# Performance work log

Hardware: AMD Instinct MI355X
Metric: run time of the kernel (lower is better)

Reference implementation:

```python
import jax, jax.numpy as jnp
import numpy as np
from jax import lax

TOP_K = 8

B, S, D, N, R = 32, 128, 512, 131072, 16


def setup_inputs() -> dict:
    key = jax.random.key(0)
    ks = jax.random.split(key, 10)
    return {
        "query": jax.random.normal(ks[0], (B, S, D), jnp.float32),
        "base_memory": jax.random.normal(ks[1], (N, D), jnp.float32) * 0.01,
        "lora_A": jax.random.normal(ks[2], (N, R), jnp.float32) * 0.01,
        "lora_B": jax.random.normal(ks[3], (R, D), jnp.float32) * 0.01,
        "gru_w_ih": jax.random.normal(ks[4], (3 * D, D), jnp.float32) * 0.02,
        "gru_w_hh": jax.random.normal(ks[5], (3 * D, D), jnp.float32) * 0.02,
        "gru_b_ih": jax.random.normal(ks[6], (3 * D,), jnp.float32) * 0.02,
        "gru_b_hh": jax.random.normal(ks[7], (3 * D,), jnpp.float32) if False else jax.random.normal(ks[7], (3 * D,), jnp.float32) * 0.02,
        "wg_w": jax.random.normal(ks[8], (1, D), jnp.float32) * 0.02,
        "wg_b": jnp.zeros((1,), jnp.float32),
    }


def gru_cell(x, h, w_ih, w_hh, b_ih, b_hh):
    # torch.nn.GRUCell math; gates ordered [r, z, n]
    gx = x @ w_ih.T + b_ih            # [B, 3D]
    gh = h @ w_hh.T + b_hh            # [B, 3D]
    gx_r, gx_z, gx_n = jnp.split(gx, 3, axis=-1)
    gh_r, gh_z, gh_n = jnp.split(gh, 3, axis=-1)
    r = jax.nn.sigmoid(gx_r + gh_r)
    z = jax.nn.sigmoid(gx_z + gh_z)
    n = jnp.tanh(gx_n + r * gh_n)
    return (1.0 - z) * n + z * h


def reference(query, base_memory, lora_A, lora_B, gru_w_ih, gru_w_hh, gru_b_ih, gru_b_hh, wg_w, wg_b):
    mem = base_memory + lora_A @ lora_B                 # [N, D]
    q = query.mean(axis=1)                              # [B, D]
    scores = q @ mem.T                                  # [B, N]
    top_scores, top_idx = lax.top_k(scores, TOP_K)      # [B, K]
    retrieved = mem[top_idx]                            # [B, K, D] gather

    h0 = jnp.zeros_like(q)
    hidden = gru_cell(retrieved.sum(axis=1), h0, gru_w_ih, gru_w_hh, gru_b_ih, gru_b_hh)

    write_prob = jax.nn.sigmoid(hidden @ wg_w.T + wg_b)  # [B, 1]
    value = q                                            # value[b, 0] in torch == q[b]

    # Sequential over batch (matches torch loop order); within a batch the
    # top-k indices are distinct so a vectorized scatter-set is exact.
    def step(m, inp):
        idx, p, v = inp                                  # [K], scalar, [D]
        rows = (1.0 - p) * m[idx] + p * v
        return m.at[idx].set(rows), None

    new_mem, _ = lax.scan(step, base_memory, (top_idx, write_prob[:, 0], value))
    return retrieved, hidden, new_mem
```

## Files before the change

### kernel.cpp

```cpp
#include <hip/hip_runtime.h>
#include <math.h>

#define NROWS 131072
#define DDIM  512
#define BB    32
#define SS    128
#define KK    8

__global__ __launch_bounds__(256) void k_qmean(const float* __restrict__ query,
                                               float* __restrict__ q) {
  __shared__ float part[256];
  int b  = blockIdx.x >> 3;
  int dc = blockIdx.x & 7;
  int t  = threadIdx.x;
  int lane = t & 63;
  int p    = t >> 6;
  const float* src = query + (size_t)b * SS * DDIM + (size_t)(p * 32) * DDIM
                   + dc * 64 + lane;
  float s = 0.f;
  #pragma unroll 8
  for (int i = 0; i < 32; ++i) s += src[(size_t)i * DDIM];
  part[t] = s;
  __syncthreads();
  if (t < 64) {
    float tot = part[t] + part[64 + t] + part[128 + t] + part[192 + t];
    q[b * DDIM + dc * 64 + t] = tot * (1.0f / 128.0f);
  }
}

__global__ __launch_bounds__(256) void k_memscores(const float* __restrict__ base,
                                                   const float* __restrict__ A,
                                                   const float* __restrict__ Bm,
                                                   const float* __restrict__ q,
                                                   float* __restrict__ newmem,
                                                   float* __restrict__ scores) {
  __shared__ float4 sq[4096];
  int t = threadIdx.x;
  const float4* qg = (const float4*)q;
  #pragma unroll
  for (int u = 0; u < 16; ++u) sq[u * 256 + t] = qg[u * 256 + t];
  __syncthreads();

  int r = blockIdx.x * 256 + t;

  const float* Ar = A + (size_t)r * 16;
  float av[16];
  #pragma unroll
  for (int j = 0; j < 4; ++j) {
    float4 a = *(const float4*)(Ar + 4 * j);
    av[4 * j]     = a.x; av[4 * j + 1] = a.y;
    av[4 * j + 2] = a.z; av[4 * j + 3] = a.w;
  }

  float acc[32];
  #pragma unroll
  for (int b = 0; b < 32; ++b) acc[b] = 0.f;

  const float4* brow = (const float4*)(base + (size_t)r * DDIM);
  float4*       nrow = (float4*)(newmem + (size_t)r * DDIM);

  float4 cur0 = brow[0], cur1 = brow[1], cur2 = brow[2], cur3 = brow[3];

  for (int g = 0; g < 32; ++g) {
    int nb = (g < 31) ? 4 * (g + 1) : 0;
    float4 nxt0 = brow[nb];
    float4 nxt1 = brow[nb + 1];
    float4 nxt2 = brow[nb + 2];
    float4 nxt3 = brow[nb + 3];

    #pragma unroll
    for (int j = 0; j < 4; ++j) {
      int d4 = 4 * g + j;
      float4 m = (j == 0) ? cur0 : (j == 1) ? cur1 : (j == 2) ? cur2 : cur3;
      #pragma unroll
      for (int rr = 0; rr < 16; ++rr) {
        float4 bv = *(const float4*)(Bm + rr * DDIM + 4 * d4);
        m.x += av[rr] * bv.x; m.y += av[rr] * bv.y;
        m.z += av[rr] * bv.z; m.w += av[rr] * bv.w;
      }
      nrow[d4] = m;
      #pragma unroll
      for (int b = 0; b < 32; ++b) {
        float4 qv = sq[b * 128 + d4];
        acc[b] += qv.x * m.x + qv.y * m.y + qv.z * m.z + qv.w * m.w;
      }
    }
    cur0 = nxt0; cur1 = nxt1; cur2 = nxt2; cur3 = nxt3;
  }

  #pragma unroll
  for (int b = 0; b < 32; ++b) scores[(size_t)b * NROWS + r] = acc[b];
}

__device__ __forceinline__ void insert8(float (&v)[8], int (&ix)[8], float x, int i) {
  bool better = (x > v[7]) || (x == v[7] && i < ix[7]);
  if (!better) return;
  v[7] = x; ix[7] = i;
  #pragma unroll
  for (int u = 7; u > 0; --u) {
    bool sw = (v[u] > v[u-1]) || (v[u] == v[u-1] && ix[u] < ix[u-1]);
    if (sw) {
      float tv = v[u]; v[u] = v[u-1]; v[u-1] = tv;
      int ti = ix[u]; ix[u] = ix[u-1]; ix[u-1] = ti;
    }
  }
}

__global__ __launch_bounds__(256) void k_topk1(const float* __restrict__ scores,
                                               float* __restrict__ cval,
                                               int* __restrict__ cidx) {
  __shared__ float lval[256][8]; __shared__ int lidx[256][8];
  __shared__ float mval[32][8];  __shared__ int midx[32][8];
  int b = blockIdx.x >> 4, j = blockIdx.x & 15, t = threadIdx.x;
  const float4* s4 = (const float4*)(scores + (size_t)b * NROWS + j * 8192);

  float v[8]; int ix[8];
  #pragma unroll
  for (int e = 0; e < 8; ++e) { v[e] = -1e30f; ix[e] = 0x7fffffff; }
  #pragma unroll
  for (int i = 0; i < 8; ++i) {
    int f4 = i * 256 + t;
    float4 x = s4[f4];
    int n0 = j * 8192 + f4 * 4;
    insert8(v, ix, x.x, n0);
    insert8(v, ix, x.y, n0 + 1);
    insert8(v, ix, x.z, n0 + 2);
    insert8(v, ix, x.w, n0 + 3);
  }
  #pragma unroll
  for (int e = 0; e < 8; ++e) { lval[t][e] = v[e]; lidx[t][e] = ix[e]; }
  __syncthreads();

  if (t < 32) {
    float mv[8]; int mi[8];
    #pragma unroll
    for (int e = 0; e < 8; ++e) { mv[e] = -1e30f; mi[e] = 0x7fffffff; }
    for (int u = 0; u < 8; ++u) {
      int src = t * 8 + u;
      #pragma unroll
      for (int e = 0; e < 8; ++e) insert8(mv, mi, lval[src][e], lidx[src][e]);
    }
    #pragma unroll
    for (int e = 0; e < 8; ++e) { mval[t][e] = mv[e]; midx[t][e] = mi[e]; }
  }
  __syncthreads();

  if (t == 0) {
    float mv[8]; int mi[8];
    #pragma unroll
    for (int e = 0; e < 8; ++e) { mv[e] = -1e30f; mi[e] = 0x7fffffff; }
    for (int u = 0; u < 32; ++u)
      #pragma unroll
      for (int e = 0; e < 8; ++e) insert8(mv, mi, mval[u][e], midx[u][e]);
    #pragma unroll
    for (int e = 0; e < 8; ++e) {
      cval[(b * 16 + j) * 8 + e] = mv[e];
      cidx[(b * 16 + j) * 8 + e] = mi[e];
    }
  }
}

__global__ __launch_bounds__(128) void k_gather(const float* __restrict__ mem,
                                                const float* __restrict__ cval,
                                                const int* __restrict__ cidx,
                                                int* __restrict__ topidx,
                                                float* __restrict__ retrieved,
                                                float* __restrict__ x) {
  __shared__ float scv[128]; __shared__ int sci[128];
  __shared__ int stop[8];
  int b = blockIdx.x, t = threadIdx.x;
  scv[t] = cval[b * 128 + t];
  sci[t] = cidx[b * 128 + t];
  __syncthreads();
  if (t == 0) {
    float mv[8]; int mi[8];
    #pragma unroll
    for (int e = 0; e < 8; ++e) { mv[e] = -1e30f; mi[e] = 0x7fffffff; }
    for (int u = 0; u < 128; ++u) insert8(mv, mi, scv[u], sci[u]);
    #pragma unroll
    for (int e = 0; e < 8; ++e) { stop[e] = mi[e]; topidx[b * 8 + e] = mi[e]; }
  }
  __syncthreads();

  float4 xs = make_float4(0.f, 0.f, 0.f, 0.f);
  #pragma unroll
  for (int k = 0; k < 8; ++k) {
    int row = stop[k];
    float4 vv = *(const float4*)(mem + (size_t)row * DDIM + 4 * t);
    *(float4*)(retrieved + (size_t)(b * 8 + k) * DDIM + 4 * t) = vv;
    xs.x += vv.x; xs.y += vv.y; xs.z += vv.z; xs.w += vv.w;
  }
  *(float4*)(x + (size_t)b * DDIM + 4 * t) = xs;
}

__global__ __launch_bounds__(512) void k_gru(const float* __restrict__ x,
                                             const float* __restrict__ wih,
                                             const float* __restrict__ bih,
                                             const float* __restrict__ bhh,
                                             const float* __restrict__ wgw,
                                             const float* __restrict__ wgb,
                                             float* __restrict__ hidden,
                                             float* __restrict__ pws) {
  __shared__ float sx[512];
  __shared__ float sred[8];
  int b = blockIdx.x, t = threadIdx.x;
  sx[t] = x[b * 512 + t];
  __syncthreads();
  const float* wr = wih + (size_t)t * 512;
  const float* wz = wih + (size_t)(512 + t) * 512;
  const float* wn = wih + (size_t)(1024 + t) * 512;
  float gr = 0.f, gz = 0.f, gn = 0.f;
  #pragma unroll 4
  for (int d4 = 0; d4 < 128; ++d4) {
    float4 xv = *(const float4*)(sx + 4 * d4);
    float4 a = *(const float4*)(wr + 4 * d4);
    float4 c = *(const float4*)(wz + 4 * d4);
    float4 e = *(const float4*)(wn + 4 * d4);
    gr += a.x*xv.x + a.y*xv.y + a.z*xv.z + a.w*xv.w;
    gz += c.x*xv.x + c.y*xv.y + c.z*xv.z + c.w*xv.w;
    gn += e.x*xv.x + e.y*xv.y + e.z*xv.z + e.w*xv.w;
  }
  float r = 1.f / (1.f + expf(-(gr + bih[t]        + bhh[t])));
  float z = 1.f / (1.f + expf(-(gz + bih[512 + t]  + bhh[512 + t])));
  float n = tanhf(gn + bih[1024 + t] + r * bhh[1024 + t]);
  float h = (1.f - z) * n;
  hidden[b * 512 + t] = h;

  float pw = h * wgw[t];
  #pragma unroll
  for (int off = 32; off > 0; off >>= 1) pw += __shfl_down(pw, off, 64);
  if ((t & 63) == 0) sred[t >> 6] = pw;
  __syncthreads();
  if (t == 0) {
    float ssum = 0.f;
    #pragma unroll
    for (int j = 0; j < 8; ++j) ssum += sred[j];
    pws[b] = 1.f / (1.f + expf(-(ssum + wgb[0])));
  }
}

__global__ __launch_bounds__(256) void k_scatter(float* __restrict__ newmem,
                                                 const int* __restrict__ topidx,
                                                 const float* __restrict__ pws,
                                                 const float* __restrict__ q) {
  int t = threadIdx.x;
  int d = blockIdx.x * 64 + (t & 63);
  int k0 = t >> 6;
  for (int b = 0; b < 32; ++b) {
    float p = pws[b];
    float qv = q[b * 512 + d];
    #pragma unroll
    for (int kk = 0; kk < 2; ++kk) {
      int k = k0 + kk * 4;
      int row = topidx[b * 8 + k];
      size_t off = (size_t)row * 512 + d;
      float m = __hip_atomic_load(newmem + off, __ATOMIC_RELAXED,
                                  __HIP_MEMORY_SCOPE_AGENT);
      __hip_atomic_store(newmem + off, (1.f - p) * m + p * qv,
                         __ATOMIC_RELAXED, __HIP_MEMORY_SCOPE_AGENT);
    }
    __syncthreads();
  }
}

extern "C" void kernel_launch(void* const* d_in, const int* in_sizes, int n_in,
                              void* d_out, int out_size, void* d_ws, size_t ws_size,
                              hipStream_t stream) {
  const float* query = (const float*)d_in[0];
  const float* base  = (const float*)d_in[1];
  const float* lA    = (const float*)d_in[2];
  const float* lB    = (const float*)d_in[3];
  const float* wih   = (const float*)d_in[4];
  const float* bih   = (const float*)d_in[6];
  const float* bhh   = (const float*)d_in[7];
  const float* wgw   = (const float*)d_in[8];
  const float* wgb   = (const float*)d_in[9];

  float* out = (float*)d_out;
  float* retrieved = out;
  float* hidden    = out + 131072;
  float* newmem    = out + 147456;

  float* wq  = (float*)d_ws;
  float* wsc = wq + 16384;
  float* wx  = wsc + 4194304;
  float* wp  = wx + 16384;
  int*   wti = (int*)(wp + 32);
  float* wcv = (float*)(wti + 256);
  int*   wci = (int*)(wcv + 4096);

  k_qmean    <<<256, 256, 0, stream>>>(query, wq);
  k_memscores<<<512, 256, 0, stream>>>(base, lA, lB, wq, newmem, wsc);
  k_topk1    <<<512, 256, 0, stream>>>(wsc, wcv, wci);
  k_gather   <<<32,  128, 0, stream>>>(newmem, wcv, wci, wti, retrieved, wx);
  k_gru      <<<32,  512, 0, stream>>>(wx, wih, bih, bhh, wgw, wgb, hidden, wp);
  k_scatter  <<<8,   256, 0, stream>>>(newmem, wti, wp, wq);
}
```

Before: 1.004 ms.

## Stage mem writes through LDS for coalescing, read q from global, split GRU blocks

k_memscores drops the 64KB LDS copy of q and reads q straight from global/cache, which frees LDS so two blocks can fit per CU (launch_bounds 256,2). Each 16-column chunk of mem is staged in a padded double-buffered LDS tile so the newmem stores become coalesced row-major writes instead of strided per-thread row writes, at the cost of one barrier per iteration. The GRU kernel is split into 256 blocks of 64 threads that combine their partial write-gate sums with atomicAdd. The sigmoid on that sum moves into the scatter kernel, and the qmean kernel zeroes the accumulator.

```diff
diff --git a/kernel.cpp b/kernel.cpp
--- a/kernel.cpp
+++ b/kernel.cpp
@@ -8,11 +8,13 @@
 #define KK    8
 
 __global__ __launch_bounds__(256) void k_qmean(const float* __restrict__ query,
-                                               float* __restrict__ q) {
+                                               float* __restrict__ q,
+                                               float* __restrict__ pwsum) {
   __shared__ float part[256];
   int b  = blockIdx.x >> 3;
   int dc = blockIdx.x & 7;
   int t  = threadIdx.x;
+  if (blockIdx.x == 0 && t < 32) pwsum[t] = 0.f;
   int lane = t & 63;
   int p    = t >> 6;
   const float* src = query + (size_t)b * SS * DDIM + (size_t)(p * 32) * DDIM
@@ -28,19 +30,14 @@
   }
 }
 
-__global__ __launch_bounds__(256) void k_memscores(const float* __restrict__ base,
-                                                   const float* __restrict__ A,
-                                                   const float* __restrict__ Bm,
-                                                   const float* __restrict__ q,
-                                                   float* __restrict__ newmem,
-                                                   float* __restrict__ scores) {
-  __shared__ float4 sq[4096];
+__global__ __launch_bounds__(256, 2) void k_memscores(const float* __restrict__ base,
+                                                      const float* __restrict__ A,
+                                                      const float* __restrict__ Bm,
+                                                      const float* __restrict__ q,
+                                                      float* __restrict__ newmem,
+                                                      float* __restrict__ scores) {
+  __shared__ float buf[2][256][17];
   int t = threadIdx.x;
-  const float4* qg = (const float4*)q;
-  #pragma unroll
-  for (int u = 0; u < 16; ++u) sq[u * 256 + t] = qg[u * 256 + t];
-  __syncthreads();
-
   int r = blockIdx.x * 256 + t;
 
   const float* Ar = A + (size_t)r * 16;
@@ -57,7 +54,8 @@
   for (int b = 0; b < 32; ++b) acc[b] = 0.f;
 
   const float4* brow = (const float4*)(base + (size_t)r * DDIM);
-  float4*       nrow = (float4*)(newmem + (size_t)r * DDIM);
+  const float4* qg   = (const float4*)q;
+  size_t rowbase = (size_t)blockIdx.x * 256;
 
   float4 cur0 = brow[0], cur1 = brow[1], cur2 = brow[2], cur3 = brow[3];
 
@@ -68,6 +66,21 @@
     float4 nxt2 = brow[nb + 2];
     float4 nxt3 = brow[nb + 3];
 
+    if (g > 0) {
+      int pg = g - 1, pb = pg & 1;
+      #pragma unroll
+      for (int it = 0; it < 4; ++it) {
+        int s = it * 256 + t;
+        int row = s >> 2, pp = s & 3;
+        float4 v;
+        v.x = buf[pb][row][pp * 4 + 0];
+        v.y = buf[pb][row][pp * 4 + 1];
+        v.z = buf[pb][row][pp * 4 + 2];
+        v.w = buf[pb][row][pp * 4 + 3];
+        *(float4*)(newmem + (rowbase + row) * DDIM + pg * 16 + pp * 4) = v;
+      }
+    }
+
     #pragma unroll
     for (int j = 0; j < 4; ++j) {
       int d4 = 4 * g + j;
@@ -78,14 +91,30 @@
         m.x += av[rr] * bv.x; m.y += av[rr] * bv.y;
         m.z += av[rr] * bv.z; m.w += av[rr] * bv.w;
       }
-      nrow[d4] = m;
+      buf[g & 1][t][4 * j + 0] = m.x;
+      buf[g & 1][t][4 * j + 1] = m.y;
+      buf[g & 1][t][4 * j + 2] = m.z;
+      buf[g & 1][t][4 * j + 3] = m.w;
       #pragma unroll
       for (int b = 0; b < 32; ++b) {
-        float4 qv = sq[b * 128 + d4];
+        float4 qv = qg[b * 128 + d4];
         acc[b] += qv.x * m.x + qv.y * m.y + qv.z * m.z + qv.w * m.w;
       }
     }
     cur0 = nxt0; cur1 = nxt1; cur2 = nxt2; cur3 = nxt3;
+    __syncthreads();
+  }
+
+  #pragma unroll
+  for (int it = 0; it < 4; ++it) {
+    int s = it * 256 + t;
+    int row = s >> 2, pp = s & 3;
+    float4 v;
+    v.x = buf[1][row][pp * 4 + 0];
+    v.y = buf[1][row][pp * 4 + 1];
+    v.z = buf[1][row][pp * 4 + 2];
+    v.w = buf[1][row][pp * 4 + 3];
+    *(float4*)(newmem + (rowbase + row) * DDIM + 31 * 16 + pp * 4) = v;
   }
 
   #pragma unroll
@@ -193,26 +222,24 @@
   *(float4*)(x + (size_t)b * DDIM + 4 * t) = xs;
 }
 
-__global__ __launch_bounds__(512) void k_gru(const float* __restrict__ x,
-                                             const float* __restrict__ wih,
-                                             const float* __restrict__ bih,
-                                             const float* __restrict__ bhh,
-                                             const float* __restrict__ wgw,
-                                             const float* __restrict__ wgb,
-                                             float* __restrict__ hidden,
-                                             float* __restrict__ pws) {
-  __shared__ float sx[512];
-  __shared__ float sred[8];
-  int b = blockIdx.x, t = threadIdx.x;
-  sx[t] = x[b * 512 + t];
-  __syncthreads();
+__global__ __launch_bounds__(64) void k_gru(const float* __restrict__ x,
+                                            const float* __restrict__ wih,
+                                            const float* __restrict__ bih,
+                                            const float* __restrict__ bhh,
+                                            const float* __restrict__ wgw,
+                                            float* __restrict__ hidden,
+                                            float* __restrict__ pwsum) {
+  int b     = blockIdx.x >> 3;
+  int chunk = blockIdx.x & 7;
+  int t = chunk * 64 + threadIdx.x;
+  const float* xb = x + b * 512;
   const float* wr = wih + (size_t)t * 512;
   const float* wz = wih + (size_t)(512 + t) * 512;
   const float* wn = wih + (size_t)(1024 + t) * 512;
   float gr = 0.f, gz = 0.f, gn = 0.f;
   #pragma unroll 4
   for (int d4 = 0; d4 < 128; ++d4) {
-    float4 xv = *(const float4*)(sx + 4 * d4);
+    float4 xv = *(const float4*)(xb + 4 * d4);
     float4 a = *(const float4*)(wr + 4 * d4);
     float4 c = *(const float4*)(wz + 4 * d4);
     float4 e = *(const float4*)(wn + 4 * d4);
@@ -229,25 +256,19 @@
   float pw = h * wgw[t];
   #pragma unroll
   for (int off = 32; off > 0; off >>= 1) pw += __shfl_down(pw, off, 64);
-  if ((t & 63) == 0) sred[t >> 6] = pw;
-  __syncthreads();
-  if (t == 0) {
-    float ssum = 0.f;
-    #pragma unroll
-    for (int j = 0; j < 8; ++j) ssum += sred[j];
-    pws[b] = 1.f / (1.f + expf(-(ssum + wgb[0])));
-  }
+  if (threadIdx.x == 0) atomicAdd(pwsum + b, pw);
 }
 
 __global__ __launch_bounds__(256) void k_scatter(float* __restrict__ newmem,
                                                  const int* __restrict__ topidx,
-                                                 const float* __restrict__ pws,
+                                                 const float* __restrict__ pwsum,
+                                                 const float* __restrict__ wgb,
                                                  const float* __restrict__ q) {
   int t = threadIdx.x;
   int d = blockIdx.x * 64 + (t & 63);
   int k0 = t >> 6;
   for (int b = 0; b < 32; ++b) {
-    float p = pws[b];
+    float p = 1.f / (1.f + expf(-(pwsum[b] + wgb[0])));
     float qv = q[b * 512 + d];
     #pragma unroll
     for (int kk = 0; kk < 2; ++kk) {
@@ -289,10 +310,10 @@
   float* wcv = (float*)(wti + 256);
   int*   wci = (int*)(wcv + 4096);
 
-  k_qmean    <<<256, 256, 0, stream>>>(query, wq);
+  k_qmean    <<<256, 256, 0, stream>>>(query, wq, wp);
   k_memscores<<<512, 256, 0, stream>>>(base, lA, lB, wq, newmem, wsc);
   k_topk1    <<<512, 256, 0, stream>>>(wsc, wcv, wci);
   k_gather   <<<32,  128, 0, stream>>>(newmem, wcv, wci, wti, retrieved, wx);
-  k_gru      <<<32,  512, 0, stream>>>(wx, wih, bih, bhh, wgw, wgb, hidden, wp);
-  k_scatter  <<<8,   256, 0, stream>>>(newmem, wti, wp, wq);
-}
+  k_gru      <<<256, 64,  0, stream>>>(wx, wih, bih, bhh, wgw, hidden, wp);
+  k_scatter  <<<8,   256, 0, stream>>>(newmem, wti, wp, wgb, wq);
+}
```

Measured after the change: 1.248 ms. +24.3%, slower.
